# Kernel optimization log

Hardware: AMD Instinct MI355X
Metric: run time of the kernel (lower is better)

## Reference

```python
import jax, jax.numpy as jnp
import numpy as np

B, S, D, H = 2, 2048, 1024, 16
DK = D // H


def setup_inputs() -> dict:
    key = jax.random.key(0)
    ks = jax.random.split(key, 12)
    scale = 1.0 / np.sqrt(D)
    inp = {
        "q": jax.random.normal(ks[0], (B, S, D), dtype=jnp.float32),
        "k": jax.random.normal(ks[1], (B, S, D), dtype=jnp.float32),
        "v": jax.random.normal(ks[2], (B, S, D), dtype=jnp.float32),
        "mask": jax.random.randint(ks[3], (B, 1, 1, S), 0, 2, dtype=jnp.int32),
        "Wq": jax.random.normal(ks[4], (D, D), dtype=jnp.float32) * scale,
        "bq": jnp.zeros((D,), dtype=jnp.float32),
        "Wk": jax.random.normal(ks[5], (D, D), dtype=jnp.float32) * scale,
        "bk": jnp.zeros((D,), dtype=jnp.float32),
        "Wv": jax.random.normal(ks[6], (D, D), dtype=jnp.float32) * scale,
        "bv": jnp.zeros((D,), dtype=jnp.float32),
        "Wo": jax.random.normal(ks[7], (D, D), dtype=jnp.float32) * scale,
        "bo": jnp.zeros((D,), dtype=jnp.float32),
    }
    return inp


def reference(q, k, v, mask, Wq, bq, Wk, bk, Wv, bv, Wo, bo):
    # Linear projections (torch nn.Linear: x @ W.T + b)
    query = q @ Wq.T + bq                      # [B,S,D]
    key = k @ Wk.T + bk
    value = v @ Wv.T + bv
    # split heads -> [B,H,S,DK]
    def split(x):
        return x.reshape(B, S, H, DK).transpose(0, 2, 1, 3)
    qh, kh, vh = split(query), split(key), split(value)
    # scaled dot-product attention with additive mask
    scores = jnp.einsum("bhqd,bhkd->bhqk", qh, kh) / jnp.sqrt(jnp.float32(DK))
    scores = jnp.where(mask == 0, jnp.float32(-1e9), scores)
    attn = jax.nn.softmax(scores, axis=-1)     # [B,H,S,S]
    out = jnp.einsum("bhqk,bhkd->bhqd", attn, vh)
    out = out.transpose(0, 2, 1, 3).reshape(B, S, D)
    return out @ Wo.T + bo
```

## Files before the change

kernel.cpp:

```cpp
#include <hip/hip_runtime.h>


constexpr int BB = 2;
constexpr int SS = 2048;
constexpr int DD = 1024;
constexpr int HH = 16;
constexpr int DKK = 64;

typedef float f32x4 __attribute__((ext_vector_type(4)));
typedef __bf16 bf16x8 __attribute__((ext_vector_type(8)));
typedef short s16x8 __attribute__((ext_vector_type(8)));
typedef short s16x4 __attribute__((ext_vector_type(4)));

#define DEV static __device__ __forceinline__

DEV f32x4 mfma16(s16x8 a, s16x8 b, f32x4 c) {
  return __builtin_amdgcn_mfma_f32_16x16x32_bf16(
      __builtin_bit_cast(bf16x8, a), __builtin_bit_cast(bf16x8, b), c, 0, 0, 0);
}

DEV void split1(float x, short& h, short& l) {
  unsigned u = __float_as_uint(x);
  h = (short)(u >> 16);
  float hf = __uint_as_float(u & 0xffff0000u);
  l = (short)(__float_as_uint(x - hf) >> 16);
}
DEV short f2bf_rne(float x) {
  unsigned u = __float_as_uint(x);
  return (short)((u + 0x7fffu + ((u >> 16) & 1u)) >> 16);
}
DEV unsigned cvtpk(float lo, float hi) {
  unsigned r;
  asm("v_cvt_pk_bf16_f32 %0, %1, %2" : "=v"(r) : "v"(lo), "v"(hi));
  return r;
}
DEV s16x8 load8s(const short* p) { return *(const s16x8*)p; }

DEV void gld_lds16(const short* g, short* l) {
  __builtin_amdgcn_global_load_lds(
      (const __attribute__((address_space(1))) void*)g,
      (__attribute__((address_space(3))) void*)l, 16, 0, 0);
}

DEV void split4(const float* __restrict__ X, short* __restrict__ H,
                short* __restrict__ L, int i) {
  float4 x = *(const float4*)(X + i);
  float xs[4] = {x.x, x.y, x.z, x.w};
  s16x4 h4, l4;
#pragma unroll
  for (int e = 0; e < 4; ++e) {
    short h, l;
    split1(xs[e], h, l);
    h4[e] = h;
    l4[e] = l;
  }
  *(s16x4*)(H + i) = h4;
  *(s16x4*)(L + i) = l4;
}

DEV void cast4(const float* __restrict__ X, short* __restrict__ Y, int i) {
  float4 x = *(const float4*)(X + i);
  float xs[4] = {x.x, x.y, x.z, x.w};
  s16x4 y4;
#pragma unroll
  for (int e = 0; e < 4; ++e) y4[e] = f2bf_rne(xs[e]);
  *(s16x4*)(Y + i) = y4;
}

__global__ __launch_bounds__(256) void prep(
    const float* __restrict__ Wq, short* __restrict__ Wqh, short* __restrict__ Wql,
    const float* __restrict__ Wk, short* __restrict__ Wkh, short* __restrict__ Wkl,
    const float* __restrict__ Wo, short* __restrict__ Woh, short* __restrict__ Wol,
    const float* __restrict__ Wv, short* __restrict__ Wvh,
    const float* __restrict__ q, short* __restrict__ qH, short* __restrict__ qL,
    const float* __restrict__ k, short* __restrict__ kH, short* __restrict__ kL) {
  const int bid = blockIdx.x;
  const int t = threadIdx.x;
  if (bid < 4096) {
    const int w = bid >> 10;
    const int i = ((bid & 1023) * 256 + t) * 4;
    if (w == 0) split4(Wq, Wqh, Wql, i);
    else if (w == 1) split4(Wk, Wkh, Wkl, i);
    else if (w == 2) split4(Wo, Woh, Wol, i);
    else cast4(Wv, Wvh, i);
  } else {
    const int a = (bid - 4096) >> 12;
    const int i = (((bid - 4096) & 4095) * 256 + t) * 4;
    if (a == 0) split4(q, qH, qL, i);
    else split4(k, kH, kL, i);
  }
}

__global__ __launch_bounds__(256) void cast_rne(const float* __restrict__ X,
                                                short* __restrict__ Y) {
  int i = (blockIdx.x * 256 + threadIdx.x) * 4;
  cast4(X, Y, i);
}

__global__ __launch_bounds__(256) void gemm_qk(
    const short* __restrict__ qAh, const short* __restrict__ qAl,
    const short* __restrict__ Wqh, const short* __restrict__ Wql,
    const float* __restrict__ bq, short* __restrict__ Qo,
    const short* __restrict__ kAh, const short* __restrict__ kAl,
    const short* __restrict__ Wkh, const short* __restrict__ Wkl,
    const float* __restrict__ bk, short* __restrict__ Kho,
    short* __restrict__ Klo) {
  __shared__ short lds[2][12288];

  const int tid = threadIdx.x;
  const int lane = tid & 63, wv = tid >> 6;
  const int lo16 = lane & 15, quad = lane >> 4;
  const int sel = blockIdx.x >> 9;
  const int bid = blockIdx.x & 511;
  const int m0 = (bid & 31) * 128;
  const int n0 = (bid >> 5) * 64;

  const short* Agh = sel ? kAh : qAh;
  const short* Agl = sel ? kAl : qAl;
  const short* Wgh = sel ? Wkh : Wqh;
  const short* Wgl = sel ? Wkl : Wql;
  const float* bias = sel ? bk : bq;

  f32x4 acc[2][4];
#pragma unroll
  for (int mt = 0; mt < 2; ++mt)
#pragma unroll
    for (int nt = 0; nt < 4; ++nt) acc[mt][nt] = f32x4{0.f, 0.f, 0.f, 0.f};

  const int rw = tid >> 2, qw = tid & 3;
  const int ra0 = tid >> 2, ra1 = (tid + 256) >> 2;

  auto stage = [&](int k0, int buf) {
    short* sAh = lds[buf];
    short* sAl = lds[buf] + 4096;
    short* sWh = lds[buf] + 8192;
    short* sWl = lds[buf] + 10240;
    gld_lds16(Wgh + (size_t)(n0 + rw) * DD + k0 + qw * 8, sWh + tid * 8);
    gld_lds16(Wgl + (size_t)(n0 + rw) * DD + k0 + qw * 8, sWl + tid * 8);
    gld_lds16(Agh + (size_t)(m0 + ra0) * DD + k0 + qw * 8, sAh + tid * 8);
    gld_lds16(Agh + (size_t)(m0 + ra1) * DD + k0 + qw * 8, sAh + (tid + 256) * 8);
    gld_lds16(Agl + (size_t)(m0 + ra0) * DD + k0 + qw * 8, sAl + tid * 8);
    gld_lds16(Agl + (size_t)(m0 + ra1) * DD + k0 + qw * 8, sAl + (tid + 256) * 8);
  };

  stage(0, 0);

  for (int kk = 0; kk < DD / 32; ++kk) {
    __syncthreads();
    if (kk + 1 < DD / 32) stage((kk + 1) * 32, (kk + 1) & 1);

    const short* sAh = lds[kk & 1];
    const short* sAl = lds[kk & 1] + 4096;
    const short* sWh = lds[kk & 1] + 8192;
    const short* sWl = lds[kk & 1] + 10240;

    s16x8 ah[2], al[2], wh[4], wl[4];
#pragma unroll
    for (int mt = 0; mt < 2; ++mt) {
      const int r = wv * 32 + mt * 16 + lo16;
      ah[mt] = *(const s16x8*)&sAh[r * 32 + quad * 8];
      al[mt] = *(const s16x8*)&sAl[r * 32 + quad * 8];
    }
#pragma unroll
    for (int nt = 0; nt < 4; ++nt) {
      const int r = nt * 16 + lo16;
      wh[nt] = *(const s16x8*)&sWh[r * 32 + quad * 8];
      wl[nt] = *(const s16x8*)&sWl[r * 32 + quad * 8];
    }
#pragma unroll
    for (int mt = 0; mt < 2; ++mt)
#pragma unroll
      for (int nt = 0; nt < 4; ++nt) {
        acc[mt][nt] = mfma16(ah[mt], wh[nt], acc[mt][nt]);
        acc[mt][nt] = mfma16(ah[mt], wl[nt], acc[mt][nt]);
        acc[mt][nt] = mfma16(al[mt], wh[nt], acc[mt][nt]);
      }
  }

#pragma unroll
  for (int mt = 0; mt < 2; ++mt)
#pragma unroll
    for (int nt = 0; nt < 4; ++nt) {
      const int n = n0 + nt * 16 + lo16;
      const float bv = bias[n];
#pragma unroll
      for (int r = 0; r < 4; ++r) {
        const int m = m0 + wv * 32 + mt * 16 + quad * 4 + r;
        const float val = acc[mt][nt][r] + bv;
        const int b = m >> 11, s = m & 2047;
        const int h = n >> 6, dk = n & 63;
        size_t idx = ((size_t)(b * HH + h) * SS + s) * DKK + dk;
        if (sel == 0) {
          Qo[idx] = f2bf_rne(val);
        } else {
          short hh, ll;
          split1(val, hh, ll);
          Kho[idx] = hh;
          Klo[idx] = ll;
        }
      }
    }
}

template <int SPLIT, int EPI>
__global__ __launch_bounds__(256) void gemm_tile(
    const short* __restrict__ Agh, const short* __restrict__ Agl,
    const short* __restrict__ Wgh, const short* __restrict__ Wgl,
    const float* __restrict__ bias, void* __restrict__ O1, void* __restrict__ O2) {
  __shared__ short lds[2][12288];

  const int tid = threadIdx.x;
  const int lane = tid & 63, wv = tid >> 6;
  const int lo16 = lane & 15, quad = lane >> 4;
  const int m0 = (blockIdx.x & 31) * 128;
  const int n0 = (blockIdx.x >> 5) * 64;

  f32x4 acc[2][4];
#pragma unroll
  for (int mt = 0; mt < 2; ++mt)
#pragma unroll
    for (int nt = 0; nt < 4; ++nt) acc[mt][nt] = f32x4{0.f, 0.f, 0.f, 0.f};

  const int rw = tid >> 2, qw = tid & 3;
  const int ra0 = tid >> 2, ra1 = (tid + 256) >> 2;

  auto stage = [&](int k0, int buf) {
    short* sAh = lds[buf];
    short* sAl = lds[buf] + 4096;
    short* sWh = lds[buf] + 8192;
    short* sWl = lds[buf] + 10240;
    gld_lds16(Wgh + (size_t)(n0 + rw) * DD + k0 + qw * 8, sWh + tid * 8);
    if constexpr (SPLIT)
      gld_lds16(Wgl + (size_t)(n0 + rw) * DD + k0 + qw * 8, sWl + tid * 8);
    gld_lds16(Agh + (size_t)(m0 + ra0) * DD + k0 + qw * 8, sAh + tid * 8);
    gld_lds16(Agh + (size_t)(m0 + ra1) * DD + k0 + qw * 8, sAh + (tid + 256) * 8);
    if constexpr (SPLIT) {
      gld_lds16(Agl + (size_t)(m0 + ra0) * DD + k0 + qw * 8, sAl + tid * 8);
      gld_lds16(Agl + (size_t)(m0 + ra1) * DD + k0 + qw * 8, sAl + (tid + 256) * 8);
    }
  };

  stage(0, 0);

  for (int kk = 0; kk < DD / 32; ++kk) {
    __syncthreads();
    if (kk + 1 < DD / 32) stage((kk + 1) * 32, (kk + 1) & 1);

    const short* sAh = lds[kk & 1];
    const short* sAl = lds[kk & 1] + 4096;
    const short* sWh = lds[kk & 1] + 8192;
    const short* sWl = lds[kk & 1] + 10240;

    s16x8 ah[2], al[2], wh[4], wl[4];
#pragma unroll
    for (int mt = 0; mt < 2; ++mt) {
      const int r = wv * 32 + mt * 16 + lo16;
      ah[mt] = *(const s16x8*)&sAh[r * 32 + quad * 8];
      if constexpr (SPLIT) al[mt] = *(const s16x8*)&sAl[r * 32 + quad * 8];
    }
#pragma unroll
    for (int nt = 0; nt < 4; ++nt) {
      const int r = nt * 16 + lo16;
      wh[nt] = *(const s16x8*)&sWh[r * 32 + quad * 8];
      if constexpr (SPLIT) wl[nt] = *(const s16x8*)&sWl[r * 32 + quad * 8];
    }
#pragma unroll
    for (int mt = 0; mt < 2; ++mt)
#pragma unroll
      for (int nt = 0; nt < 4; ++nt) {
        acc[mt][nt] = mfma16(ah[mt], wh[nt], acc[mt][nt]);
        if constexpr (SPLIT) {
          acc[mt][nt] = mfma16(ah[mt], wl[nt], acc[mt][nt]);
          acc[mt][nt] = mfma16(al[mt], wh[nt], acc[mt][nt]);
        }
      }
  }

#pragma unroll
  for (int mt = 0; mt < 2; ++mt)
#pragma unroll
    for (int nt = 0; nt < 4; ++nt) {
      const int n = n0 + nt * 16 + lo16;
      const float bv = bias[n];
#pragma unroll
      for (int r = 0; r < 4; ++r) {
        const int m = m0 + wv * 32 + mt * 16 + quad * 4 + r;
        const float val = acc[mt][nt][r] + bv;
        const int b = m >> 11, s = m & 2047;
        const int h = n >> 6, dk = n & 63;
        if constexpr (EPI == 1) {
          size_t idx = ((size_t)(b * HH + h) * DKK + dk) * SS + s;
          ((short*)O1)[idx] = f2bf_rne(val);
        } else {
          ((float*)O1)[(size_t)m * DD + n] = val;
        }
      }
    }
}

constexpr int PAD = 68;
constexpr int NKB = SS / 64;
constexpr float EXPSC = 0.125f * 1.4426950408889634f;

__global__ __launch_bounds__(256, 2) void mha_attn(
    const short* __restrict__ Qh, const short* __restrict__ Kh,
    const short* __restrict__ Kl, const short* __restrict__ Vt,
    const int* __restrict__ mask, short* __restrict__ Ah,
    short* __restrict__ Al) {
  __shared__ short sKh[64 * PAD];
  __shared__ short sKl[64 * PAD];
  __shared__ short sV[64 * PAD];
  __shared__ short sP[4][32 * PAD];

  const int tid = threadIdx.x;
  const int lane = tid & 63, wv = tid >> 6;
  const int lo16 = lane & 15, quad = lane >> 4;
  const int bid = blockIdx.x;
  const int head = (bid & 7) * 4 + ((bid >> 3) & 3);
  const int qblk = bid >> 5;
  const int q0 = qblk * 128 + wv * 32;
  const int b = head >> 4;

  const size_t hbase = (size_t)head * SS;

  constexpr short ONE_BF = (short)0x3F80;
  const s16x8 ones8 = {ONE_BF, ONE_BF, ONE_BF, ONE_BF,
                       ONE_BF, ONE_BF, ONE_BF, ONE_BF};

  s16x8 qh[2][2];
#pragma unroll
  for (int rt = 0; rt < 2; ++rt) {
    size_t qb = (hbase + q0 + rt * 16 + lo16) * DKK + quad * 8;
#pragma unroll
    for (int c = 0; c < 2; ++c) qh[rt][c] = load8s(Qh + qb + c * 32);
  }

  f32x4 Oacc[2][4];
#pragma unroll
  for (int rt = 0; rt < 2; ++rt)
#pragma unroll
    for (int t = 0; t < 4; ++t) Oacc[rt][t] = f32x4{0.f, 0.f, 0.f, 0.f};
  f32x4 sacc[2];
  sacc[0] = f32x4{0.f, 0.f, 0.f, 0.f};
  sacc[1] = f32x4{0.f, 0.f, 0.f, 0.f};

  const int srow = tid >> 2;
  const int scol0 = (tid & 3) * 8;

  s16x8 rKh[2], rKl[2], rV[2];
#pragma unroll
  for (int i = 0; i < 2; ++i) {
    const int sc_ = scol0 + i * 32;
    rKh[i] = load8s(Kh + (hbase + srow) * DKK + sc_);
    rKl[i] = load8s(Kl + (hbase + srow) * DKK + sc_);
    rV[i] = load8s(Vt + ((size_t)head * DKK + srow) * SS + sc_);
  }

  for (int kb = 0; kb < NKB; ++kb) {
    const int k0g = kb * 64;
#pragma unroll
    for (int i = 0; i < 2; ++i) {
      const int sc_ = scol0 + i * 32;
      *(s16x8*)&sKh[srow * PAD + sc_] = rKh[i];
      *(s16x8*)&sKl[srow * PAD + sc_] = rKl[i];
      *(s16x8*)&sV[srow * PAD + sc_] = rV[i];
    }
    __syncthreads();

    if (kb + 1 < NKB) {
      const int k0n = k0g + 64;
#pragma unroll
      for (int i = 0; i < 2; ++i) {
        const int sc_ = scol0 + i * 32;
        rKh[i] = load8s(Kh + (hbase + k0n + srow) * DKK + sc_);
        rKl[i] = load8s(Kl + (hbase + k0n + srow) * DKK + sc_);
        rV[i] = load8s(Vt + ((size_t)head * DKK + srow) * SS + k0n + sc_);
      }
    }

    float addf[4][4];
#pragma unroll
    for (int sub = 0; sub < 4; ++sub) {
      const int4 mq = *(const int4*)(mask + b * SS + k0g + sub * 16 + quad * 4);
      addf[sub][0] = mq.x ? 0.f : -32768.f;
      addf[sub][1] = mq.y ? 0.f : -32768.f;
      addf[sub][2] = mq.z ? 0.f : -32768.f;
      addf[sub][3] = mq.w ? 0.f : -32768.f;
    }

    f32x4 sc4[2][4];
    __builtin_amdgcn_s_setprio(1);
#pragma unroll
    for (int sub = 0; sub < 4; ++sub) {
      sc4[0][sub] = f32x4{0.f, 0.f, 0.f, 0.f};
      sc4[1][sub] = f32x4{0.f, 0.f, 0.f, 0.f};
      const int krow = sub * 16 + lo16;
#pragma unroll
      for (int c = 0; c < 2; ++c) {
        s16x8 kh = *(const s16x8*)&sKh[krow * PAD + c * 32 + quad * 8];
        s16x8 kl = *(const s16x8*)&sKl[krow * PAD + c * 32 + quad * 8];
#pragma unroll
        for (int rt = 0; rt < 2; ++rt) {
          sc4[rt][sub] = mfma16(kh, qh[rt][c], sc4[rt][sub]);
          sc4[rt][sub] = mfma16(kl, qh[rt][c], sc4[rt][sub]);
        }
      }
    }
    __builtin_amdgcn_s_setprio(0);

#pragma unroll
    for (int rt = 0; rt < 2; ++rt) {
      const int prow = (rt * 16 + lo16) * PAD;
#pragma unroll
      for (int sub = 0; sub < 4; ++sub) {
        const float p0 = exp2f(fmaf(sc4[rt][sub][0], EXPSC, addf[sub][0]));
        const float p1 = exp2f(fmaf(sc4[rt][sub][1], EXPSC, addf[sub][1]));
        const float p2 = exp2f(fmaf(sc4[rt][sub][2], EXPSC, addf[sub][2]));
        const float p3 = exp2f(fmaf(sc4[rt][sub][3], EXPSC, addf[sub][3]));
        *(unsigned*)&sP[wv][prow + sub * 16 + quad * 4] = cvtpk(p0, p1);
        *(unsigned*)&sP[wv][prow + sub * 16 + quad * 4 + 2] = cvtpk(p2, p3);
      }
    }

    s16x8 pa[2][2];
#pragma unroll
    for (int rt = 0; rt < 2; ++rt)
#pragma unroll
      for (int c = 0; c < 2; ++c)
        pa[rt][c] = *(const s16x8*)&sP[wv][(rt * 16 + lo16) * PAD + c * 32 + quad * 8];
    __builtin_amdgcn_s_setprio(1);
#pragma unroll
    for (int rt = 0; rt < 2; ++rt) {
      sacc[rt] = mfma16(pa[rt][0], ones8, sacc[rt]);
      sacc[rt] = mfma16(pa[rt][1], ones8, sacc[rt]);
    }
#pragma unroll
    for (int t = 0; t < 4; ++t)
#pragma unroll
      for (int c = 0; c < 2; ++c) {
        s16x8 vb = *(const s16x8*)&sV[(t * 16 + lo16) * PAD + c * 32 + quad * 8];
#pragma unroll
        for (int rt = 0; rt < 2; ++rt)
          Oacc[rt][t] = mfma16(pa[rt][c], vb, Oacc[rt][t]);
      }
    __builtin_amdgcn_s_setprio(0);
    __syncthreads();
  }

  const int h = head & 15;
#pragma unroll
  for (int rt = 0; rt < 2; ++rt) {
#pragma unroll
    for (int r = 0; r < 4; ++r) {
      const float rinv = 1.0f / sacc[rt][r];
#pragma unroll
      for (int t = 0; t < 4; ++t) {
        const float val = Oacc[rt][t][r] * rinv;
        const int row = q0 + rt * 16 + quad * 4 + r;
        const int col = h * DKK + t * 16 + lo16;
        const size_t idx = ((size_t)b * SS + row) * DD + col;
        short hh, ll;
        split1(val, hh, ll);
        Ah[idx] = hh;
        Al[idx] = ll;
      }
    }
  }
}

extern "C" void kernel_launch(void* const* d_in, const int* in_sizes, int n_in,
                              void* d_out, int out_size, void* d_ws, size_t ws_size,
                              hipStream_t stream) {
  const float* q = (const float*)d_in[0];
  const float* k = (const float*)d_in[1];
  const float* v = (const float*)d_in[2];
  const int* mask = (const int*)d_in[3];
  const float* Wq = (const float*)d_in[4];
  const float* bq = (const float*)d_in[5];
  const float* Wk = (const float*)d_in[6];
  const float* bk = (const float*)d_in[7];
  const float* Wv = (const float*)d_in[8];
  const float* bv = (const float*)d_in[9];
  const float* Wo = (const float*)d_in[10];
  const float* bo = (const float*)d_in[11];

  char* ws = (char*)d_ws;
  size_t off = 0;
  auto take = [&](size_t bytes) {
    char* p = ws + off;
    off += (bytes + 255) & ~(size_t)255;
    return p;
  };
  const size_t WE = (size_t)DD * DD;
  const size_t TE = (size_t)BB * SS * DD;

  short* Wqh = (short*)take(WE * 2);
  short* Wql = (short*)take(WE * 2);
  short* Wkh = (short*)take(WE * 2);
  short* Wkl = (short*)take(WE * 2);
  short* Wvh = (short*)take(WE * 2);
  short* Woh = (short*)take(WE * 2);
  short* Wol = (short*)take(WE * 2);
  short* qH = (short*)take(TE * 2);
  short* qL = (short*)take(TE * 2);
  short* kH = (short*)take(TE * 2);
  short* kL = (short*)take(TE * 2);
  short* Qh = (short*)take(TE * 2);
  short* Kh = (short*)take(TE * 2);
  short* Kl = (short*)take(TE * 2);
  (void)ws_size;
  short* vH = qH;
  short* Vt = qL;
  short* aH = kH;
  short* aL = kL;

  prep<<<12288, 256, 0, stream>>>(Wq, Wqh, Wql, Wk, Wkh, Wkl, Wo, Woh, Wol,
                                  Wv, Wvh, q, qH, qL, k, kH, kL);

  gemm_qk<<<1024, 256, 0, stream>>>(qH, qL, Wqh, Wql, bq, Qh,
                                    kH, kL, Wkh, Wkl, bk, Kh, Kl);

  cast_rne<<<4096, 256, 0, stream>>>(v, vH);
  gemm_tile<0, 1><<<512, 256, 0, stream>>>(vH, nullptr, Wvh, nullptr, bv, Vt, nullptr);

  mha_attn<<<512, 256, 0, stream>>>(Qh, Kh, Kl, Vt, mask, aH, aL);

  gemm_tile<1, 2><<<512, 256, 0, stream>>>(aH, aL, Woh, Wol, bo, d_out, nullptr);
}
```

Measured before the change: 318.5 us.

## Double-buffer attention K/V tiles via direct global-to-LDS loads with XOR swizzle

The attention kernel now stages K-high, K-low and V tiles straight from global memory into a double-buffered LDS array using gld_lds16, instead of going through registers and padded LDS. The projection epilogues write K and V^T in an XOR-swizzled layout, so the unpadded 64-wide LDS rows can be read with few bank conflicts. One __syncthreads per iteration is dropped. This is meant to cut register pressure and overlap the next tile's loads with compute. The cost is a larger LDS footprint, which may lower occupancy, and the correctness of the remaining single barrier depends on gld_lds completion semantics.

```diff
diff --git a/kernel.cpp b/kernel.cpp
--- a/kernel.cpp
+++ b/kernel.cpp
@@ -189,10 +189,12 @@
         const float val = acc[mt][nt][r] + bv;
         const int b = m >> 11, s = m & 2047;
         const int h = n >> 6, dk = n & 63;
-        size_t idx = ((size_t)(b * HH + h) * SS + s) * DKK + dk;
         if (sel == 0) {
+          size_t idx = ((size_t)(b * HH + h) * SS + s) * DKK + dk;
           Qo[idx] = f2bf_rne(val);
         } else {
+          const int dk_sw = dk ^ ((s & 7) << 3);
+          size_t idx = ((size_t)(b * HH + h) * SS + s) * DKK + dk_sw;
           short hh, ll;
           split1(val, hh, ll);
           Kho[idx] = hh;
@@ -289,7 +291,8 @@
         const int b = m >> 11, s = m & 2047;
         const int h = n >> 6, dk = n & 63;
         if constexpr (EPI == 1) {
-          size_t idx = ((size_t)(b * HH + h) * DKK + dk) * SS + s;
+          const int s_sw = s ^ ((dk & 7) << 3);
+          size_t idx = ((size_t)(b * HH + h) * DKK + dk) * SS + s_sw;
           ((short*)O1)[idx] = f2bf_rne(val);
         } else {
           ((float*)O1)[(size_t)m * DD + n] = val;
@@ -307,9 +310,7 @@
     const short* __restrict__ Kl, const short* __restrict__ Vt,
     const int* __restrict__ mask, short* __restrict__ Ah,
     short* __restrict__ Al) {
-  __shared__ short sKh[64 * PAD];
-  __shared__ short sKl[64 * PAD];
-  __shared__ short sV[64 * PAD];
+  __shared__ short sKV[2][12288];
   __shared__ short sP[4][32 * PAD];
 
   const int tid = threadIdx.x;
@@ -322,6 +323,7 @@
   const int b = head >> 4;
 
   const size_t hbase = (size_t)head * SS;
+  const size_t vbase = (size_t)head * DKK;
 
   constexpr short ONE_BF = (short)0x3F80;
   const s16x8 ones8 = {ONE_BF, ONE_BF, ONE_BF, ONE_BF,
@@ -344,39 +346,31 @@
   sacc[0] = f32x4{0.f, 0.f, 0.f, 0.f};
   sacc[1] = f32x4{0.f, 0.f, 0.f, 0.f};
 
-  const int srow = tid >> 2;
-  const int scol0 = (tid & 3) * 8;
-
-  s16x8 rKh[2], rKl[2], rV[2];
-#pragma unroll
-  for (int i = 0; i < 2; ++i) {
-    const int sc_ = scol0 + i * 32;
-    rKh[i] = load8s(Kh + (hbase + srow) * DKK + sc_);
-    rKl[i] = load8s(Kl + (hbase + srow) * DKK + sc_);
-    rV[i] = load8s(Vt + ((size_t)head * DKK + srow) * SS + sc_);
-  }
+  auto STAGE = [&](int k0, int buf) {
+    short* base = &sKV[buf][0];
+#pragma unroll
+    for (int i = 0; i < 2; ++i) {
+      const int ch = tid + 256 * i;
+      const int row = ch >> 3;
+      const int inner = (ch & 7) * 8;
+      gld_lds16(Kh + (hbase + k0 + row) * DKK + inner, base + ch * 8);
+      gld_lds16(Kl + (hbase + k0 + row) * DKK + inner, base + 4096 + ch * 8);
+      gld_lds16(Vt + (vbase + row) * SS + k0 + inner, base + 8192 + ch * 8);
+    }
+  };
+
+  STAGE(0, 0);
 
   for (int kb = 0; kb < NKB; ++kb) {
     const int k0g = kb * 64;
-#pragma unroll
-    for (int i = 0; i < 2; ++i) {
-      const int sc_ = scol0 + i * 32;
-      *(s16x8*)&sKh[srow * PAD + sc_] = rKh[i];
-      *(s16x8*)&sKl[srow * PAD + sc_] = rKl[i];
-      *(s16x8*)&sV[srow * PAD + sc_] = rV[i];
-    }
+    const int cur = kb & 1;
     __syncthreads();
 
-    if (kb + 1 < NKB) {
-      const int k0n = k0g + 64;
-#pragma unroll
-      for (int i = 0; i < 2; ++i) {
-        const int sc_ = scol0 + i * 32;
-        rKh[i] = load8s(Kh + (hbase + k0n + srow) * DKK + sc_);
-        rKl[i] = load8s(Kl + (hbase + k0n + srow) * DKK + sc_);
-        rV[i] = load8s(Vt + ((size_t)head * DKK + srow) * SS + k0n + sc_);
-      }
-    }
+    if (kb + 1 < NKB) STAGE(k0g + 64, cur ^ 1);
+
+    const short* sKh = &sKV[cur][0];
+    const short* sKl = &sKV[cur][4096];
+    const short* sV = &sKV[cur][8192];
 
     float addf[4][4];
 #pragma unroll
@@ -395,10 +389,12 @@
       sc4[0][sub] = f32x4{0.f, 0.f, 0.f, 0.f};
       sc4[1][sub] = f32x4{0.f, 0.f, 0.f, 0.f};
       const int krow = sub * 16 + lo16;
+      const int ksw = (krow & 7) << 3;
 #pragma unroll
       for (int c = 0; c < 2; ++c) {
-        s16x8 kh = *(const s16x8*)&sKh[krow * PAD + c * 32 + quad * 8];
-        s16x8 kl = *(const s16x8*)&sKl[krow * PAD + c * 32 + quad * 8];
+        const int koff = krow * 64 + ((c * 32 + quad * 8) ^ ksw);
+        s16x8 kh = *(const s16x8*)&sKh[koff];
+        s16x8 kl = *(const s16x8*)&sKl[koff];
 #pragma unroll
         for (int rt = 0; rt < 2; ++rt) {
           sc4[rt][sub] = mfma16(kh, qh[rt][c], sc4[rt][sub]);
@@ -435,16 +431,18 @@
       sacc[rt] = mfma16(pa[rt][1], ones8, sacc[rt]);
     }
 #pragma unroll
-    for (int t = 0; t < 4; ++t)
+    for (int t = 0; t < 4; ++t) {
+      const int vrow = t * 16 + lo16;
+      const int vsw = (vrow & 7) << 3;
 #pragma unroll
       for (int c = 0; c < 2; ++c) {
-        s16x8 vb = *(const s16x8*)&sV[(t * 16 + lo16) * PAD + c * 32 + quad * 8];
+        s16x8 vb = *(const s16x8*)&sV[vrow * 64 + ((c * 32 + quad * 8) ^ vsw)];
 #pragma unroll
         for (int rt = 0; rt < 2; ++rt)
           Oacc[rt][t] = mfma16(pa[rt][c], vb, Oacc[rt][t]);
       }
+    }
     __builtin_amdgcn_s_setprio(0);
-    __syncthreads();
   }
 
   const int h = head & 15;
```

Measured after the change: 312.6 us. About the same (-1.8%).
